# Kernel optimization log

Measured on AMD Instinct MI355X. Metric: run time of the kernel, lower is better.

Reference implementation:

```python
import jax, jax.numpy as jnp
import numpy as np

BATCH = 4096
INDIM = 1024
OUTDIM = 1024
NNZ = 52224  # min(1024,1024) * int(1024 * 0.05)


def setup_inputs() -> dict:
    key = jax.random.key(0)
    k1, k2, k3, k4, k5 = jax.random.split(key, 5)
    stdv = np.sqrt(2.0 / INDIM).astype(np.float32)
    input_ = jax.random.normal(k1, (BATCH, INDIM), dtype=jnp.float32)
    weight = jax.random.normal(k2, (NNZ,), dtype=jnp.float32) * stdv
    bias = jax.random.normal(k3, (OUTDIM,), dtype=jnp.float32) * stdv
    ind_in = jax.random.randint(k4, (NNZ,), 0, INDIM, dtype=jnp.int32)
    ind_out = jax.random.randint(k5, (NNZ,), 0, OUTDIM, dtype=jnp.int32)
    return {"input_": input_, "weight": weight, "bias": bias,
            "ind_in": ind_in, "ind_out": ind_out}


def reference(input_, weight, bias, ind_in, ind_out):
    # x = input_[:, ind_in] * weight        [B, NNZ]
    gathered = input_[:, ind_in] * weight
    # scatter_add into output columns       [B, OUTDIM]
    out = jnp.zeros((input_.shape[0], OUTDIM), dtype=input_.dtype)
    out = out.at[:, ind_out].add(gathered)
    return out + bias
```

## Files before the change

kernel.cpp:

```cpp
#include <hip/hip_runtime.h>
#include <stdint.h>

#define INDIM   1024
#define OUTDIM  1024
#define BTILE   16
#define SLAB_U32 12
#define ELL_MAX 128


__global__ void k_scatter(const int* __restrict__ ind_in, const int* __restrict__ ind_out,
                          const float* __restrict__ w, int* __restrict__ cursor,
                          int2* __restrict__ ell, int nnz) {
    int k = blockIdx.x * 256 + threadIdx.x;
    if (k < nnz) {
        int o = ind_out[k];
        int pos = atomicAdd(&cursor[o], 1);
        if (pos < ELL_MAX) {
            int2 e;
            e.x = ind_in[k] * (SLAB_U32 * 4);
            e.y = __float_as_int(w[k]);
            ell[(size_t)pos * OUTDIM + o] = e;
        }
    }
}


#define FMA8E(f, W)                                                             \
    acc[0] = fmaf(__uint_as_float((f).x << 16),          (W), acc[0]);          \
    acc[1] = fmaf(__uint_as_float((f).x & 0xFFFF0000u),  (W), acc[1]);          \
    acc[2] = fmaf(__uint_as_float((f).y << 16),          (W), acc[2]);          \
    acc[3] = fmaf(__uint_as_float((f).y & 0xFFFF0000u),  (W), acc[3]);          \
    acc[4] = fmaf(__uint_as_float((f).z << 16),          (W), acc[4]);          \
    acc[5] = fmaf(__uint_as_float((f).z & 0xFFFF0000u),  (W), acc[5]);          \
    acc[6] = fmaf(__uint_as_float((f).w << 16),          (W), acc[6]);          \
    acc[7] = fmaf(__uint_as_float((f).w & 0xFFFF0000u),  (W), acc[7]);

__device__ __forceinline__ uint32_t bf16pack(float x, float y) {
    uint32_t ux = __float_as_uint(x);
    ux = ((ux + 0x7FFFu + ((ux >> 16) & 1u)) >> 16) & 0xFFFFu;
    uint32_t uy = __float_as_uint(y);
    uy = (uy + 0x7FFFu + ((uy >> 16) & 1u)) & 0xFFFF0000u;
    return ux | uy;
}

__global__ __launch_bounds__(1024, 4) void k_spmm(
    const float* __restrict__ in, const int2* __restrict__ ell,
    const int* __restrict__ cnt, const float* __restrict__ bias,
    float* __restrict__ out)
{
    __shared__ uint32_t slab[INDIM * SLAB_U32];

    const int t  = threadIdx.x;
    const int b0 = blockIdx.x * BTILE;

    {
        const float* colp = in + (size_t)b0 * INDIM + t;
        #pragma unroll
        for (int r = 0; r < 8; r++) {
            float v0 = colp[(size_t)(2 * r)     * INDIM];
            float v1 = colp[(size_t)(2 * r + 1) * INDIM];
            slab[t * SLAB_U32 + r] = bf16pack(v0, v1);
        }
    }
    __syncthreads();

    const int boct = t & 1;
    const int og   = t >> 1;
    const int boff = boct * 16;
    const char* slab_b = (const char*)slab;

    for (int j = 0; j < 2; j++) {
        const int o  = og + 512 * j;
        const int n  = cnt[o];
        const int2* ep = ell + o;
        float acc[8] = {0.f, 0.f, 0.f, 0.f, 0.f, 0.f, 0.f, 0.f};

        int k = 0;
        for (; k + 2 <= n; k += 2) {
            int2 e0 = ep[(size_t)k * OUTDIM];
            int2 e1 = ep[(size_t)(k + 1) * OUTDIM];
            uint4 f0 = *(const uint4*)(slab_b + e0.x + boff);
            uint4 f1 = *(const uint4*)(slab_b + e1.x + boff);
            float w0 = __int_as_float(e0.y);
            float w1 = __int_as_float(e1.y);
            FMA8E(f0, w0);
            FMA8E(f1, w1);
        }
        if (k < n) {
            int2 e0 = ep[(size_t)k * OUTDIM];
            uint4 f0 = *(const uint4*)(slab_b + e0.x + boff);
            float w0 = __int_as_float(e0.y);
            FMA8E(f0, w0);
        }

        const float bv = bias[o];
        float* op = out + (size_t)(b0 + boct * 8) * OUTDIM + o;
        #pragma unroll
        for (int e = 0; e < 8; e++) op[(size_t)e * OUTDIM] = acc[e] + bv;
    }
}


extern "C" void kernel_launch(void* const* d_in, const int* in_sizes, int n_in,
                              void* d_out, int out_size, void* d_ws, size_t ws_size,
                              hipStream_t stream) {
    const float* input  = (const float*)d_in[0];
    const float* weight = (const float*)d_in[1];
    const float* bias   = (const float*)d_in[2];
    const int*   ind_in  = (const int*)d_in[3];
    const int*   ind_out = (const int*)d_in[4];
    float* out = (float*)d_out;

    const int nnz   = in_sizes[1];
    const int batch = out_size / OUTDIM;

    char* ws = (char*)d_ws;
    int*  cursor = (int*)ws;
    int2* ell    = (int2*)(ws + 4096);

    (void)hipMemsetAsync(cursor, 0, OUTDIM * sizeof(int), stream);
    k_scatter<<<(nnz + 255) / 256, 256, 0, stream>>>(ind_in, ind_out, weight, cursor, ell, nnz);
    k_spmm<<<batch / BTILE, 1024, 0, stream>>>(input, ell, cursor, bias, out);
}
```

Measured before the change: 112.1 us.

## Densify sparse weight and compute output with bf16 MFMA GEMM

Replaces the ELL-format sparse gather/FMA kernel with three steps: scatter-add the sparse weights into a dense transposed fp32 weight matrix, convert input and weight to bf16, then run a tiled 128x128x64 MFMA GEMM with bias added in the epilogue. The aim is to swap irregular LDS gathers and scalar FMAs for dense matrix-core throughput, at the price of about twenty times more arithmetic. It also adds a 4 MB memset, an atomic scatter and a conversion pass over both matrices. Rounding the weights to bf16 costs some accuracy compared with the fp32 weights used before.

Result: slower. 132.5 us (+18.1%).

```diff
diff --git a/kernel.cpp b/kernel.cpp
--- a/kernel.cpp
+++ b/kernel.cpp
@@ -3,37 +3,20 @@
 
 #define INDIM   1024
 #define OUTDIM  1024
-#define BTILE   16
-#define SLAB_U32 12
-#define ELL_MAX 128
+#define BM 128
+#define BN 128
+#define BK 64
+#define KTILES (INDIM / BK)
 
+typedef __attribute__((ext_vector_type(8))) short  short8;
+typedef __attribute__((ext_vector_type(4))) float  floatx4;
 
-__global__ void k_scatter(const int* __restrict__ ind_in, const int* __restrict__ ind_out,
-                          const float* __restrict__ w, int* __restrict__ cursor,
-                          int2* __restrict__ ell, int nnz) {
+__global__ void k_scatter_w(const int* __restrict__ ind_in, const int* __restrict__ ind_out,
+                            const float* __restrict__ w, float* __restrict__ W32T, int nnz) {
     int k = blockIdx.x * 256 + threadIdx.x;
-    if (k < nnz) {
-        int o = ind_out[k];
-        int pos = atomicAdd(&cursor[o], 1);
-        if (pos < ELL_MAX) {
-            int2 e;
-            e.x = ind_in[k] * (SLAB_U32 * 4);
-            e.y = __float_as_int(w[k]);
-            ell[(size_t)pos * OUTDIM + o] = e;
-        }
-    }
+    if (k < nnz)
+        atomicAdd(&W32T[(size_t)ind_out[k] * INDIM + ind_in[k]], w[k]);
 }
-
-
-#define FMA8E(f, W)                                                             \
-    acc[0] = fmaf(__uint_as_float((f).x << 16),          (W), acc[0]);          \
-    acc[1] = fmaf(__uint_as_float((f).x & 0xFFFF0000u),  (W), acc[1]);          \
-    acc[2] = fmaf(__uint_as_float((f).y << 16),          (W), acc[2]);          \
-    acc[3] = fmaf(__uint_as_float((f).y & 0xFFFF0000u),  (W), acc[3]);          \
-    acc[4] = fmaf(__uint_as_float((f).z << 16),          (W), acc[4]);          \
-    acc[5] = fmaf(__uint_as_float((f).z & 0xFFFF0000u),  (W), acc[5]);          \
-    acc[6] = fmaf(__uint_as_float((f).w << 16),          (W), acc[6]);          \
-    acc[7] = fmaf(__uint_as_float((f).w & 0xFFFF0000u),  (W), acc[7]);
 
 __device__ __forceinline__ uint32_t bf16pack(float x, float y) {
     uint32_t ux = __float_as_uint(x);
@@ -43,63 +26,102 @@
     return ux | uy;
 }
 
-__global__ __launch_bounds__(1024, 4) void k_spmm(
-    const float* __restrict__ in, const int2* __restrict__ ell,
-    const int* __restrict__ cnt, const float* __restrict__ bias,
-    float* __restrict__ out)
-{
-    __shared__ uint32_t slab[INDIM * SLAB_U32];
-
-    const int t  = threadIdx.x;
-    const int b0 = blockIdx.x * BTILE;
-
-    {
-        const float* colp = in + (size_t)b0 * INDIM + t;
-        #pragma unroll
-        for (int r = 0; r < 8; r++) {
-            float v0 = colp[(size_t)(2 * r)     * INDIM];
-            float v1 = colp[(size_t)(2 * r + 1) * INDIM];
-            slab[t * SLAB_U32 + r] = bf16pack(v0, v1);
-        }
+__global__ void k_convert(const float4* __restrict__ A, uint2* __restrict__ A16, int nA4,
+                          const float4* __restrict__ Wt, uint2* __restrict__ W16, int nW4) {
+    int i = blockIdx.x * 256 + threadIdx.x;
+    int stride = gridDim.x * 256;
+    for (int j = i; j < nA4; j += stride) {
+        float4 v = A[j];
+        A16[j] = make_uint2(bf16pack(v.x, v.y), bf16pack(v.z, v.w));
     }
-    __syncthreads();
-
-    const int boct = t & 1;
-    const int og   = t >> 1;
-    const int boff = boct * 16;
-    const char* slab_b = (const char*)slab;
-
-    for (int j = 0; j < 2; j++) {
-        const int o  = og + 512 * j;
-        const int n  = cnt[o];
-        const int2* ep = ell + o;
-        float acc[8] = {0.f, 0.f, 0.f, 0.f, 0.f, 0.f, 0.f, 0.f};
-
-        int k = 0;
-        for (; k + 2 <= n; k += 2) {
-            int2 e0 = ep[(size_t)k * OUTDIM];
-            int2 e1 = ep[(size_t)(k + 1) * OUTDIM];
-            uint4 f0 = *(const uint4*)(slab_b + e0.x + boff);
-            uint4 f1 = *(const uint4*)(slab_b + e1.x + boff);
-            float w0 = __int_as_float(e0.y);
-            float w1 = __int_as_float(e1.y);
-            FMA8E(f0, w0);
-            FMA8E(f1, w1);
-        }
-        if (k < n) {
-            int2 e0 = ep[(size_t)k * OUTDIM];
-            uint4 f0 = *(const uint4*)(slab_b + e0.x + boff);
-            float w0 = __int_as_float(e0.y);
-            FMA8E(f0, w0);
-        }
-
-        const float bv = bias[o];
-        float* op = out + (size_t)(b0 + boct * 8) * OUTDIM + o;
-        #pragma unroll
-        for (int e = 0; e < 8; e++) op[(size_t)e * OUTDIM] = acc[e] + bv;
+    for (int j = i; j < nW4; j += stride) {
+        float4 v = Wt[j];
+        W16[j] = make_uint2(bf16pack(v.x, v.y), bf16pack(v.z, v.w));
     }
 }
 
+__global__ __launch_bounds__(256) void k_gemm(
+    const ushort* __restrict__ A16,
+    const ushort* __restrict__ W16T,
+    const float* __restrict__ bias,
+    float* __restrict__ C, int M)
+{
+    __shared__ ushort lA[BM * BK];
+    __shared__ ushort lB[BN * BK];
+
+    const int t      = threadIdx.x;
+    const int w      = t >> 6;
+    const int L      = t & 63;
+    const int lane15 = L & 15;
+    const int lane7  = L & 7;
+    const int quad   = L >> 4;
+    const int wm     = w >> 1, wn = w & 1;
+
+    const int bm0 = (blockIdx.x >> 3) * BM;
+    const int bn0 = (blockIdx.x & 7) * BN;
+
+    const int srow_base = w * 32 + (L >> 3);
+    const int j8g       = (L & 7) ^ (L >> 3);
+    const int cbase     = w * 256 + L;
+
+    const ushort* Abase = A16  + (size_t)bm0 * INDIM;
+    const ushort* Bbase = W16T + (size_t)bn0 * INDIM;
+
+    floatx4 acc[4][4] = {};
+
+    for (int kt = 0; kt < KTILES; ++kt) {
+        uint4 va[4], vb[4];
+        #pragma unroll
+        for (int q = 0; q < 4; ++q) {
+            const size_t goff = (size_t)(srow_base + q * 8) * INDIM + kt * BK + j8g * 8;
+            va[q] = *(const uint4*)(Abase + goff);
+            vb[q] = *(const uint4*)(Bbase + goff);
+        }
+        __syncthreads();
+        #pragma unroll
+        for (int q = 0; q < 4; ++q) {
+            *(uint4*)(lA + (size_t)(cbase + q * 64) * 8) = va[q];
+            *(uint4*)(lB + (size_t)(cbase + q * 64) * 8) = vb[q];
+        }
+        __syncthreads();
+
+        #pragma unroll
+        for (int ks = 0; ks < 2; ++ks) {
+            const int koff = (((ks * 4 + quad) ^ lane7) * 8);
+            short8 af[4], bf[4];
+            #pragma unroll
+            for (int tm = 0; tm < 4; ++tm)
+                af[tm] = *(const short8*)(lA + (wm * 64 + tm * 16 + lane15) * 64 + koff);
+            #pragma unroll
+            for (int tn = 0; tn < 4; ++tn)
+                bf[tn] = *(const short8*)(lB + (wn * 64 + tn * 16 + lane15) * 64 + koff);
+            #pragma unroll
+            for (int tm = 0; tm < 4; ++tm)
+                #pragma unroll
+                for (int tn = 0; tn < 4; ++tn)
+                    acc[tm][tn] = __builtin_amdgcn_mfma_f32_16x16x32_bf16(
+                        af[tm], bf[tn], acc[tm][tn], 0, 0, 0);
+        }
+    }
+
+    float bv[4];
+    #pragma unroll
+    for (int tn = 0; tn < 4; ++tn)
+        bv[tn] = bias[bn0 + wn * 64 + tn * 16 + lane15];
+
+    #pragma unroll
+    for (int tm = 0; tm < 4; ++tm) {
+        #pragma unroll
+        for (int tn = 0; tn < 4; ++tn) {
+            const int col = bn0 + wn * 64 + tn * 16 + lane15;
+            #pragma unroll
+            for (int r = 0; r < 4; ++r) {
+                const int row = bm0 + wm * 64 + tm * 16 + quad * 4 + r;
+                C[(size_t)row * OUTDIM + col] = acc[tm][tn][r] + bv[tn];
+            }
+        }
+    }
+}
 
 extern "C" void kernel_launch(void* const* d_in, const int* in_sizes, int n_in,
                               void* d_out, int out_size, void* d_ws, size_t ws_size,
@@ -111,14 +133,17 @@
     const int*   ind_out = (const int*)d_in[4];
     float* out = (float*)d_out;
 
-    const int nnz   = in_sizes[1];
-    const int batch = out_size / OUTDIM;
+    const int nnz = in_sizes[1];
+    const int M   = out_size / OUTDIM;
 
     char* ws = (char*)d_ws;
-    int*  cursor = (int*)ws;
-    int2* ell    = (int2*)(ws + 4096);
+    float*  W32T = (float*)ws;
+    ushort* W16T = (ushort*)(ws + (4u << 20));
+    ushort* A16  = (ushort*)(ws + (6u << 20));
 
-    (void)hipMemsetAsync(cursor, 0, OUTDIM * sizeof(int), stream);
-    k_scatter<<<(nnz + 255) / 256, 256, 0, stream>>>(ind_in, ind_out, weight, cursor, ell, nnz);
-    k_spmm<<<batch / BTILE, 1024, 0, stream>>>(input, ell, cursor, bias, out);
+    (void)hipMemsetAsync(W32T, 0, (size_t)OUTDIM * INDIM * sizeof(float), stream);
+    k_scatter_w<<<(nnz + 255) / 256, 256, 0, stream>>>(ind_in, ind_out, weight, W32T, nnz);
+    k_convert<<<2048, 256, 0, stream>>>((const float4*)input, (uint2*)A16, M * INDIM / 4,
+                                        (const float4*)W32T, (uint2*)W16T, OUTDIM * INDIM / 4);
+    k_gemm<<<(M / BM) * (OUTDIM / BN), 256, 0, stream>>>(A16, W16T, bias, out, M);
 }
```
